# Optimization experiments

Measured on AMD Instinct MI355X. Metric: run time of the kernel, lower is better.

Reference implementation:

```python
import jax, jax.numpy as jnp
import numpy as np

B, T, I, R, O = 1, 2048, 8, 4096, 8
SPECTRAL_RADIUS = 0.9
SPARSITY = 0.1


def setup_inputs() -> dict:
    key = jax.random.key(0)
    k1, k2, k3, k4, k5, k6 = jax.random.split(key, 6)
    x = jax.random.normal(k1, (B, T, I), dtype=jnp.float32)
    Win = jax.random.normal(k2, (R, I), dtype=jnp.float32)
    W = jax.random.normal(k3, (R, R), dtype=jnp.float32)
    # sparse mask + spectral-radius scaling (circular-law approx: rho(sparse gaussian) ~ sqrt(sparsity*R))
    mask = (jax.random.uniform(k4, (R, R)) < SPARSITY).astype(jnp.float32)
    W = W * mask * (SPECTRAL_RADIUS / jnp.sqrt(SPARSITY * R))
    Wout_w = jax.random.normal(k5, (O, R), dtype=jnp.float32) / jnp.sqrt(R)
    Wout_b = jax.random.normal(k6, (O,), dtype=jnp.float32) * 0.01
    return {"x": x, "Win": Win, "W": W, "Wout_w": Wout_w, "Wout_b": Wout_b}


def reference(x, Win, W, Wout_w, Wout_b):
    Bb = x.shape[0]
    h0 = jnp.zeros((Bb, W.shape[0]), dtype=x.dtype)

    def step(h, xt):  # xt: [B, I]
        h = jnp.tanh(xt @ Win.T + h @ W.T)          # [B, R]
        out = h @ Wout_w.T + Wout_b                  # [B, O]
        return h, out

    xs = jnp.swapaxes(x, 0, 1)                       # [T, B, I]
    _, outs = jax.lax.scan(step, h0, xs)             # outs: [T, B, O]
    return jnp.swapaxes(outs, 0, 1)                  # [B, T, O]
```

## Files before the change

### kernel.cpp

```cpp
#include <hip/hip_runtime.h>
#include <math.h>


#define T_STEPS 2048
#define R_DIM   4096
#define I_DIM   8
#define O_DIM   8
#define NWG     128
#define ROWS_PER_WG (R_DIM / NWG)
#define POOL_CAP 16384
#define BLOCK    512

typedef float v4f __attribute__((ext_vector_type(4)));

__device__ float        g_hist[(size_t)T_STEPS * R_DIM];
__device__ unsigned int g_flag[NWG * 32];

__global__ void esn_init_kernel() {
    for (int i = threadIdx.x; i < NWG * 32; i += blockDim.x)
        __hip_atomic_store(&g_flag[i], 0u, __ATOMIC_RELAXED,
                           __HIP_MEMORY_SCOPE_SYSTEM);
}

__launch_bounds__(BLOCK, 1)
__global__ void esn_recur_kernel(const float* __restrict__ x,
                                 const float* __restrict__ Win,
                                 const float* __restrict__ W) {
    __shared__ uint2 s_pool[POOL_CAP];
    __shared__ float s_h[R_DIM];
    __shared__ int   s_start[ROWS_PER_WG + 1];
    __shared__ int   s_cnt[ROWS_PER_WG];
    __shared__ float s_win[ROWS_PER_WG][I_DIM];

    const int wg   = blockIdx.x;
    const int tid  = threadIdx.x;
    const int lane = tid & 63;
    const int wave = tid >> 6;
    const int row0 = wg * ROWS_PER_WG;

    for (int rr = wave; rr < ROWS_PER_WG; rr += 8) {
        const float* wrow = W + (size_t)(row0 + rr) * R_DIM;
        int cnt = 0;
        for (int base = 0; base < R_DIM; base += 64) {
            float v = wrow[base + lane];
            cnt += __popcll(__ballot(v != 0.0f));
        }
        if (lane == 0) s_cnt[rr] = cnt;
    }
    __syncthreads();
    if (tid == 0) {
        int acc = 0;
        for (int rr = 0; rr < ROWS_PER_WG; ++rr) {
            s_start[rr] = (acc < POOL_CAP) ? acc : POOL_CAP;
            acc += s_cnt[rr];
        }
        s_start[ROWS_PER_WG] = (acc < POOL_CAP) ? acc : POOL_CAP;
    }
    __syncthreads();
    for (int rr = wave; rr < ROWS_PER_WG; rr += 8) {
        const float* wrow = W + (size_t)(row0 + rr) * R_DIM;
        int off = s_start[rr];
        for (int base = 0; base < R_DIM; base += 64) {
            float v = wrow[base + lane];
            unsigned long long m = __ballot(v != 0.0f);
            int pre = __popcll(m & ((1ull << lane) - 1ull));
            if (v != 0.0f) {
                int pos = off + pre;
                if (pos < POOL_CAP) {
                    s_pool[pos].x = __float_as_uint(v);
                    s_pool[pos].y = base + lane;
                }
            }
            off += __popcll(m);
        }
    }
    if (tid < ROWS_PER_WG * I_DIM) {
        int rr = tid / I_DIM, c = tid % I_DIM;
        s_win[rr][c] = Win[(size_t)(row0 + rr) * I_DIM + c];
    }
    __syncthreads();

    const int row16 = tid >> 4;
    const int sub   = tid & 15;
    const int start = s_start[row16];
    const int cnt   = s_start[row16 + 1] - start;

    for (int t = 0; t < T_STEPS; ++t) {
        if (t > 0) {
            const unsigned ut = (unsigned)t;
            if (tid < NWG) {
                while (__hip_atomic_load(&g_flag[tid << 5], __ATOMIC_RELAXED,
                                         __HIP_MEMORY_SCOPE_SYSTEM) < ut)
                    __builtin_amdgcn_s_sleep(2);
            }
            __syncthreads();
            const v4f* src = (const v4f*)(g_hist + (size_t)(t - 1) * R_DIM);
            v4f r0, r1;
            const v4f* a0 = src + tid;
            const v4f* a1 = src + tid + 512;
            asm volatile(
                "global_load_dwordx4 %0, %2, off sc0 sc1\n\t"
                "global_load_dwordx4 %1, %3, off sc0 sc1\n\t"
                "s_waitcnt vmcnt(0)"
                : "=v"(r0), "=v"(r1)
                : "v"(a0), "v"(a1)
                : "memory");
            v4f* dst = (v4f*)s_h;
            dst[tid]       = r0;
            dst[tid + 512] = r1;
            __syncthreads();
        }

        float acc = 0.0f;
        if (t > 0) {
            for (int e = start + sub; e < start + cnt; e += 16) {
                uint2 p = s_pool[e];
                acc += __uint_as_float(p.x) * s_h[p.y];
            }
        }
        acc += __shfl_xor(acc, 8, 16);
        acc += __shfl_xor(acc, 4, 16);
        acc += __shfl_xor(acc, 2, 16);
        acc += __shfl_xor(acc, 1, 16);

        if (sub == 0) {
            const float* xt = x + (size_t)t * I_DIM;
            float a = acc;
            #pragma unroll
            for (int c = 0; c < I_DIM; ++c) a += s_win[row16][c] * xt[c];
            float h = tanhf(a);
            __hip_atomic_store(&g_hist[(size_t)t * R_DIM + row0 + row16], h,
                               __ATOMIC_RELAXED, __HIP_MEMORY_SCOPE_SYSTEM);
        }
        asm volatile("s_waitcnt vmcnt(0)" ::: "memory");
        __syncthreads();
        if (tid == 0)
            __hip_atomic_store(&g_flag[wg << 5], (unsigned)(t + 1),
                               __ATOMIC_RELAXED, __HIP_MEMORY_SCOPE_SYSTEM);
    }
}

__global__ void esn_out_kernel(const float* __restrict__ Wout_w,
                               const float* __restrict__ Wout_b,
                               float* __restrict__ out) {
    const int t = blockIdx.x;
    const int lane = threadIdx.x;
    const float* hp = g_hist + (size_t)t * R_DIM;
    float acc[O_DIM];
    #pragma unroll
    for (int o = 0; o < O_DIM; ++o) acc[o] = 0.0f;
    for (int i = lane; i < R_DIM; i += 256) {
        float h0 = __hip_atomic_load(hp + i,       __ATOMIC_RELAXED, __HIP_MEMORY_SCOPE_SYSTEM);
        float h1 = __hip_atomic_load(hp + i + 64,  __ATOMIC_RELAXED, __HIP_MEMORY_SCOPE_SYSTEM);
        float h2 = __hip_atomic_load(hp + i + 128, __ATOMIC_RELAXED, __HIP_MEMORY_SCOPE_SYSTEM);
        float h3 = __hip_atomic_load(hp + i + 192, __ATOMIC_RELAXED, __HIP_MEMORY_SCOPE_SYSTEM);
        #pragma unroll
        for (int o = 0; o < O_DIM; ++o) acc[o] += h0 * Wout_w[(size_t)o * R_DIM + i];
        #pragma unroll
        for (int o = 0; o < O_DIM; ++o) acc[o] += h1 * Wout_w[(size_t)o * R_DIM + i + 64];
        #pragma unroll
        for (int o = 0; o < O_DIM; ++o) acc[o] += h2 * Wout_w[(size_t)o * R_DIM + i + 128];
        #pragma unroll
        for (int o = 0; o < O_DIM; ++o) acc[o] += h3 * Wout_w[(size_t)o * R_DIM + i + 192];
    }
    #pragma unroll
    for (int o = 0; o < O_DIM; ++o) {
        float a = acc[o];
        a += __shfl_xor(a, 32);
        a += __shfl_xor(a, 16);
        a += __shfl_xor(a, 8);
        a += __shfl_xor(a, 4);
        a += __shfl_xor(a, 2);
        a += __shfl_xor(a, 1);
        if (lane == 0) out[(size_t)t * O_DIM + o] = a + Wout_b[o];
    }
}

extern "C" void kernel_launch(void* const* d_in, const int* in_sizes, int n_in,
                              void* d_out, int out_size, void* d_ws, size_t ws_size,
                              hipStream_t stream) {
    const float* x    = (const float*)d_in[0];
    const float* Win  = (const float*)d_in[1];
    const float* W    = (const float*)d_in[2];
    const float* Ww   = (const float*)d_in[3];
    const float* Wb   = (const float*)d_in[4];
    float* out = (float*)d_out;

    hipLaunchKernelGGL(esn_init_kernel, dim3(1), dim3(256), 0, stream);

    void* args[] = { (void*)&x, (void*)&Win, (void*)&W };
    hipLaunchCooperativeKernel((void*)esn_recur_kernel, dim3(NWG), dim3(BLOCK),
                               args, 0, stream);

    hipLaunchKernelGGL(esn_out_kernel, dim3(T_STEPS), dim3(64), 0, stream,
                       Ww, Wb, out);
}
```

Before: 8.808 ms.

## Poll producer flags per wave and drop the pre-load block barrier

Each wave now polls only the 16 producer workgroup flags whose hidden-state slice it will copy into shared memory, using a wave-wide vote. This replaces the single group of 128 pollers followed by a block-wide barrier. Each thread now loads a contiguous 32-byte chunk instead of two strided 16-byte chunks. The per-step input vector is loaded as two float4s at the top of the step, ahead of the wait. The aim is to shorten the critical path of each recurrence step by removing one barrier and overlapping the x load with the wait, at the cost of more flag-polling traffic across waves.

```diff
diff --git a/kernel.cpp b/kernel.cpp
--- a/kernel.cpp
+++ b/kernel.cpp
@@ -85,29 +85,38 @@
     const int start = s_start[row16];
     const int cnt   = s_start[row16 + 1] - start;
 
+    const int  src_wg  = (wave << 4) + (lane & 15);
+    const bool poller  = (lane < 16);
+    const unsigned* fp = &g_flag[src_wg << 5];
+
     for (int t = 0; t < T_STEPS; ++t) {
+        const float4* xp = (const float4*)(x + (size_t)t * I_DIM);
+        const float4 xa = xp[0];
+        const float4 xb = xp[1];
+
         if (t > 0) {
             const unsigned ut = (unsigned)t;
-            if (tid < NWG) {
-                while (__hip_atomic_load(&g_flag[tid << 5], __ATOMIC_RELAXED,
-                                         __HIP_MEMORY_SCOPE_SYSTEM) < ut)
-                    __builtin_amdgcn_s_sleep(2);
+            for (;;) {
+                unsigned v = poller
+                    ? __hip_atomic_load(fp, __ATOMIC_RELAXED,
+                                        __HIP_MEMORY_SCOPE_SYSTEM)
+                    : ut;
+                if (__all(v >= ut)) break;
+                __builtin_amdgcn_s_sleep(1);
             }
-            __syncthreads();
-            const v4f* src = (const v4f*)(g_hist + (size_t)(t - 1) * R_DIM);
+            const v4f* bp = (const v4f*)(g_hist + (size_t)(t - 1) * R_DIM
+                                         + (size_t)tid * 8);
             v4f r0, r1;
-            const v4f* a0 = src + tid;
-            const v4f* a1 = src + tid + 512;
             asm volatile(
                 "global_load_dwordx4 %0, %2, off sc0 sc1\n\t"
-                "global_load_dwordx4 %1, %3, off sc0 sc1\n\t"
+                "global_load_dwordx4 %1, %2, off offset:16 sc0 sc1\n\t"
                 "s_waitcnt vmcnt(0)"
                 : "=v"(r0), "=v"(r1)
-                : "v"(a0), "v"(a1)
+                : "v"(bp)
                 : "memory");
-            v4f* dst = (v4f*)s_h;
-            dst[tid]       = r0;
-            dst[tid + 512] = r1;
+            v4f* dst = (v4f*)(s_h + (size_t)tid * 8);
+            dst[0] = r0;
+            dst[1] = r1;
             __syncthreads();
         }
 
@@ -124,10 +133,15 @@
         acc += __shfl_xor(acc, 1, 16);
 
         if (sub == 0) {
-            const float* xt = x + (size_t)t * I_DIM;
             float a = acc;
-            #pragma unroll
-            for (int c = 0; c < I_DIM; ++c) a += s_win[row16][c] * xt[c];
+            a += s_win[row16][0] * xa.x;
+            a += s_win[row16][1] * xa.y;
+            a += s_win[row16][2] * xa.z;
+            a += s_win[row16][3] * xa.w;
+            a += s_win[row16][4] * xb.x;
+            a += s_win[row16][5] * xb.y;
+            a += s_win[row16][6] * xb.z;
+            a += s_win[row16][7] * xb.w;
             float h = tanhf(a);
             __hip_atomic_store(&g_hist[(size_t)t * R_DIM + row0 + row16], h,
                                __ATOMIC_RELAXED, __HIP_MEMORY_SCOPE_SYSTEM);
```

Result: faster. 8.600 ms (-2.4%).
